# Kernel tuning notes

Measured on AMD Instinct MI355X. Metric: run time of the kernel, lower is better.

Reference implementation:

```python
import jax, jax.numpy as jnp
import numpy as np
from jax import lax

SCALE = 4          # pansharpening ratio (init arg)
K = 31             # kornia BoxBlur((31,31))
PAD = K // 2
EPS = 1e-10
R_EXP = 4          # r in the paper
A_W = 1.0          # a weight on loss_a


def box_blur(x):
    # x: [B,1,H,W]; normalized 31x31 box filter with reflect padding
    # (kornia BoxBlur default border_type='reflect'), done separably.
    xp = jnp.pad(x, ((0, 0), (0, 0), (PAD, PAD), (PAD, PAD)), mode='reflect')
    kv = jnp.ones((1, 1, K, 1), x.dtype) / K
    kh = jnp.ones((1, 1, 1, K), x.dtype) / K
    dn = ('NCHW', 'OIHW', 'NCHW')
    y = lax.conv_general_dilated(xp, kv, (1, 1), 'VALID', dimension_numbers=dn)
    return lax.conv_general_dilated(y, kh, (1, 1), 'VALID', dimension_numbers=dn)


def setup_inputs() -> dict:
    key = jax.random.key(0)
    k1, k2, k3, k4 = jax.random.split(key, 4)
    B, C, H, W = 4, 8, 1024, 1024
    h, w = H // SCALE, W // SCALE
    return {
        'lr_ms':   jax.random.uniform(k1, (B, C, h, w), jnp.float32),
        'hr_pan':  jax.random.uniform(k2, (B, 1, H, W), jnp.float32),
        'hr_ms':   jax.random.uniform(k3, (B, C, H, W), jnp.float32),
        'fuse_ms': jax.random.uniform(k4, (B, C, H, W), jnp.float32),
    }


def reference(lr_ms, hr_pan, hr_ms, fuse_ms):
    B, C, h, w = lr_ms.shape
    H, W = hr_pan.shape[2], hr_pan.shape[3]

    # F.upsample(mode='area', scale_factor=1/SCALE) == SCALE x SCALE average pool
    dp = hr_pan.reshape(B, 1, H // SCALE, SCALE, W // SCALE, SCALE).mean(axis=(3, 5))
    b = dp.reshape(B, -1)                                   # [B, N]

    # Batched lstsq: A = [1, lr_ms bands]^T per sample, solve via normal eqs
    ones = jnp.ones((B, 1, h * w), lr_ms.dtype)
    A = jnp.concatenate([ones, lr_ms.reshape(B, C, -1)], axis=1)   # [B, C+1, N]
    AtA = jnp.einsum('bcn,bdn->bcd', A, A)                  # [B, C+1, C+1]
    Atb = jnp.einsum('bcn,bn->bc', A, b)                    # [B, C+1]
    sol = jnp.linalg.solve(AtA, Atb[..., None])[..., 0]     # [B, C+1]

    # Synthetic intensity images M_ (from GT hr_ms) and G_ (from fused output)
    bias = sol[:, 0][:, None, None]
    M_ = (bias + jnp.einsum('bc,bchw->bhw', sol[:, 1:], hr_ms))[:, None]    # [B,1,H,W]
    G_ = (bias + jnp.einsum('bc,bchw->bhw', sol[:, 1:], fuse_ms))[:, None]  # [B,1,H,W]

    mean_M = box_blur(M_)
    mean_P = box_blur(hr_pan)
    cov_MP = box_blur(M_ * hr_pan) - mean_M * mean_P
    std_M = jnp.sqrt(jnp.abs(box_blur(M_ * M_) - mean_M * mean_M) + EPS)
    std_P = jnp.sqrt(jnp.abs(box_blur(hr_pan * hr_pan) - mean_P * mean_P) + EPS)
    S = (cov_MP / (std_M * std_P)) ** R_EXP                 # [B,1,H,W], broadcasts over C

    loss_c = jnp.mean(jnp.abs(fuse_ms * S - hr_ms * S))

    grad_P = (hr_pan - mean_P) / std_P
    mean_G = box_blur(G_)
    std_G = jnp.sqrt(jnp.abs(box_blur(G_ * G_) - mean_G * mean_G) + EPS)
    grad_G = (G_ - mean_G) / std_G
    loss_a = jnp.mean(jnp.abs(grad_G * (2 - S) - grad_P * (2 - S)))

    return loss_c + A_W * loss_a
```

## Files before the change

### kernel.cpp

```cpp
#include <hip/hip_runtime.h>
#include <math.h>

#define HW_IMG (1u<<20)
#define W_ 1024
#define H_ 1024
#define B_ 4
#define C_ 8
#define N_LR 65536

__device__ __forceinline__ int refl1024(int i){
  if(i<0) i=-i;
  if(i>1023) i=2046-i;
  return i;
}

__global__ __launch_bounds__(256) void k_fit(const float* __restrict__ lr_ms,
                                             const float* __restrict__ hr_pan,
                                             double* __restrict__ atab){
  int b = blockIdx.y;
  int tid = blockIdx.x*256 + threadIdx.x;
  float acc[54];
  #pragma unroll
  for(int i=0;i<54;i++) acc[i]=0.f;
  const float* pan = hr_pan + (size_t)b*HW_IMG;
  const float* lr  = lr_ms + (size_t)b*C_*N_LR;
  for(int k=0;k<4;k++){
    int n = tid*4+k;
    int i = n>>8, j = n&255;
    float s=0.f;
    #pragma unroll
    for(int dy=0;dy<4;dy++){
      const float* pr = pan + (size_t)(i*4+dy)*W_ + j*4;
      s += pr[0]+pr[1]+pr[2]+pr[3];
    }
    float bv = s*(1.f/16.f);
    float a[9];
    a[0]=1.f;
    #pragma unroll
    for(int c=0;c<C_;c++) a[c+1]=lr[(size_t)c*N_LR + n];
    int idx=0;
    #pragma unroll
    for(int p=0;p<9;p++){
      #pragma unroll
      for(int q=p;q<9;q++){ acc[idx] = fmaf(a[p],a[q],acc[idx]); idx++; }
    }
    #pragma unroll
    for(int p=0;p<9;p++) acc[45+p] = fmaf(a[p],bv,acc[45+p]);
  }
  #pragma unroll
  for(int v=0;v<54;v++){
    float x = acc[v];
    for(int off=32;off>0;off>>=1) x += __shfl_down(x, off, 64);
    if((threadIdx.x & 63)==0) atomicAdd(&atab[b*54+v], (double)x);
  }
}

__global__ void k_solve(const double* __restrict__ atab, double* __restrict__ sol){
  int b = threadIdx.x;
  if(b>=B_) return;
  double A[9][10];
  const double* src = atab + b*54;
  int idx=0;
  for(int p=0;p<9;p++)
    for(int q=p;q<9;q++){ A[p][q]=src[idx]; A[q][p]=src[idx]; idx++; }
  for(int p=0;p<9;p++) A[p][9]=src[45+p];
  for(int col=0; col<9; col++){
    int piv=col; double mx=fabs(A[col][col]);
    for(int r=col+1;r<9;r++){ double v=fabs(A[r][col]); if(v>mx){mx=v;piv=r;} }
    if(piv!=col){
      for(int c2=col;c2<10;c2++){ double t=A[col][c2]; A[col][c2]=A[piv][c2]; A[piv][c2]=t; }
    }
    double inv = 1.0/A[col][col];
    for(int r=col+1;r<9;r++){
      double f = A[r][col]*inv;
      for(int c2=col;c2<10;c2++) A[r][c2] -= f*A[col][c2];
    }
  }
  double x[9];
  for(int r=8;r>=0;r--){
    double s=A[r][9];
    for(int c2=r+1;c2<9;c2++) s -= A[r][c2]*x[c2];
    x[r]=s/A[r][r];
  }
  for(int i=0;i<9;i++) sol[b*9+i]=x[i];
}

__global__ __launch_bounds__(256) void k_synth(const float* __restrict__ hr_ms,
                                               const float* __restrict__ fuse_ms,
                                               const double* __restrict__ sol,
                                               float* __restrict__ M,
                                               float* __restrict__ G,
                                               float* __restrict__ D){
  size_t t = (size_t)blockIdx.x*256 + threadIdx.x;
  int b = (int)(t >> 18);
  size_t pix = (t & (size_t)((1<<18)-1))*4;
  const double* s = sol + b*9;
  float bias = (float)s[0];
  float4 m = {bias,bias,bias,bias};
  float4 g = m;
  float4 d = {0.f,0.f,0.f,0.f};
  #pragma unroll
  for(int c=0;c<C_;c++){
    float w = (float)s[c+1];
    size_t off = (((size_t)b*C_ + c)<<20) + pix;
    float4 hv = *(const float4*)(hr_ms+off);
    float4 fv = *(const float4*)(fuse_ms+off);
    m.x=fmaf(w,hv.x,m.x); m.y=fmaf(w,hv.y,m.y); m.z=fmaf(w,hv.z,m.z); m.w=fmaf(w,hv.w,m.w);
    g.x=fmaf(w,fv.x,g.x); g.y=fmaf(w,fv.y,g.y); g.z=fmaf(w,fv.z,g.z); g.w=fmaf(w,fv.w,g.w);
    d.x+=fabsf(fv.x-hv.x); d.y+=fabsf(fv.y-hv.y); d.z+=fabsf(fv.z-hv.z); d.w+=fabsf(fv.w-hv.w);
  }
  size_t p = ((size_t)b<<20) + pix;
  *(float4*)(M+p)=m; *(float4*)(G+p)=g; *(float4*)(D+p)=d;
}

__global__ __launch_bounds__(256) void k_vblur(const float* __restrict__ M,
                                               const float* __restrict__ P,
                                               const float* __restrict__ G,
                                               float* __restrict__ VB){
  int x  = blockIdx.x*256 + threadIdx.x;
  int b  = blockIdx.y;
  int y0 = blockIdx.z * 16;
  const float* Mp = M + (size_t)b*HW_IMG;
  const float* Pp = P + (size_t)b*HW_IMG;
  const float* Gp = G + (size_t)b*HW_IMG;
  float S0=0,S1=0,S2=0,S3=0,S4=0,S5=0,S6=0;
  #define TAPV(yy, op) { int r = refl1024(yy); size_t off=(size_t)r*W_+x; \
    float mv=Mp[off], pv=Pp[off], gv=Gp[off]; \
    S0 op mv; S1 op pv; S2 op mv*pv; S3 op mv*mv; S4 op pv*pv; S5 op gv; S6 op gv*gv; }
  for(int k=y0-15;k<=y0+15;k++) TAPV(k, +=);
  const float inv = 1.f/31.f;
  size_t base = (size_t)b*HW_IMG + (size_t)y0*W_ + x;
  const size_t CH = (size_t)B_*HW_IMG;
  for(int i=0;i<16;i++){
    size_t o = base + (size_t)i*W_;
    VB[o]      = S0*inv; VB[CH+o]   = S1*inv; VB[2*CH+o] = S2*inv;
    VB[3*CH+o] = S3*inv; VB[4*CH+o] = S4*inv; VB[5*CH+o] = S5*inv;
    VB[6*CH+o] = S6*inv;
    if(i<15){
      int y = y0+i;
      TAPV(y+16, +=);
      TAPV(y-15, -=);
    }
  }
  #undef TAPV
}

#define LIDX(i) ((i)+((i)>>5))
__global__ __launch_bounds__(128) void k_hfinal(const float* __restrict__ VB,
                                                const float* __restrict__ P,
                                                const float* __restrict__ G,
                                                const float* __restrict__ D,
                                                double* __restrict__ partial){
  __shared__ float lds[7*1056];
  __shared__ float red[4];
  int row = blockIdx.x;
  int b = row>>10, y = row&1023;
  int t = threadIdx.x;
  size_t rowoff = (size_t)b*HW_IMG + (size_t)y*W_;
  const size_t CH = (size_t)B_*HW_IMG;
  for(int ch=0; ch<7; ch++){
    const float* src = VB + (size_t)ch*CH + rowoff;
    float* dst = lds + ch*1056;
    for(int i=t*4; i<1024; i+=512){
      float4 v = *(const float4*)(src+i);
      dst[LIDX(i)]   = v.x;
      dst[LIDX(i+1)] = v.y;
      dst[LIDX(i+2)] = v.z;
      dst[LIDX(i+3)] = v.w;
    }
  }
  int x0 = t*8;
  float pv[8], gv[8], dv[8];
  {
    const float* Pr = P + rowoff + x0;
    const float* Gr = G + rowoff + x0;
    const float* Dr = D + rowoff + x0;
    #pragma unroll
    for(int i=0;i<2;i++){
      float4 a = *(const float4*)(Pr + i*4);
      pv[i*4]=a.x; pv[i*4+1]=a.y; pv[i*4+2]=a.z; pv[i*4+3]=a.w;
      float4 c = *(const float4*)(Gr + i*4);
      gv[i*4]=c.x; gv[i*4+1]=c.y; gv[i*4+2]=c.z; gv[i*4+3]=c.w;
      float4 e = *(const float4*)(Dr + i*4);
      dv[i*4]=e.x; dv[i*4+1]=e.y; dv[i*4+2]=e.z; dv[i*4+3]=e.w;
    }
  }
  __syncthreads();
  float S[7];
  #pragma unroll
  for(int ch=0;ch<7;ch++) S[ch]=0.f;
  #define TAPH(xx, op) { int r=refl1024(xx); int li=LIDX(r); \
    S[0] op lds[li];        S[1] op lds[1056+li];   S[2] op lds[2*1056+li]; \
    S[3] op lds[3*1056+li]; S[4] op lds[4*1056+li]; S[5] op lds[5*1056+li]; \
    S[6] op lds[6*1056+li]; }
  for(int k=x0-15;k<=x0+15;k++) TAPH(k, +=);
  const float inv = 1.f/31.f;
  float lc=0.f, la=0.f;
  #pragma unroll
  for(int i=0;i<8;i++){
    float mM=S[0]*inv, mP=S[1]*inv, mMP=S[2]*inv, mMM=S[3]*inv,
          mPP=S[4]*inv, mG=S[5]*inv, mGG=S[6]*inv;
    float cov  = mMP - mM*mP;
    float stdM = sqrtf(fabsf(mMM - mM*mM)+1e-10f);
    float stdP = sqrtf(fabsf(mPP - mP*mP)+1e-10f);
    float stdG = sqrtf(fabsf(mGG - mG*mG)+1e-10f);
    float corr = cov/(stdM*stdP);
    float c2 = corr*corr;
    float S4v = c2*c2;
    float gradP = (pv[i]-mP)/stdP;
    float gradG = (gv[i]-mG)/stdG;
    lc += dv[i]*S4v;
    la += fabsf((gradG-gradP)*(2.f-S4v));
    if(i<7){
      int x = x0+i;
      TAPH(x+16, +=);
      TAPH(x-15, -=);
    }
  }
  #undef TAPH
  for(int off=32;off>0;off>>=1){
    lc += __shfl_down(lc, off, 64);
    la += __shfl_down(la, off, 64);
  }
  int wid = t>>6;
  if((t&63)==0){ red[wid*2]=lc; red[wid*2+1]=la; }
  __syncthreads();
  if(t==0){
    partial[(size_t)row*2]   = (double)red[0]+(double)red[2];
    partial[(size_t)row*2+1] = (double)red[1]+(double)red[3];
  }
}

__global__ __launch_bounds__(256) void k_out(const double* __restrict__ partial,
                                             float* __restrict__ out){
  int t = threadIdx.x;
  double lc=0.0, la=0.0;
  for(int i=t;i<4096;i+=256){ lc+=partial[2*i]; la+=partial[2*i+1]; }
  for(int off=32;off>0;off>>=1){
    lc += __shfl_down(lc, off, 64);
    la += __shfl_down(la, off, 64);
  }
  __shared__ double red[8];
  int wid = t>>6;
  if((t&63)==0){ red[wid*2]=lc; red[wid*2+1]=la; }
  __syncthreads();
  if(t==0){
    double c = red[0]+red[2]+red[4]+red[6];
    double a = red[1]+red[3]+red[5]+red[7];
    out[0] = (float)(c*(1.0/33554432.0) + a*(1.0/4194304.0));
  }
}

extern "C" void kernel_launch(void* const* d_in, const int* in_sizes, int n_in,
                              void* d_out, int out_size, void* d_ws, size_t ws_size,
                              hipStream_t stream){
  const float* lr_ms   = (const float*)d_in[0];
  const float* hr_pan  = (const float*)d_in[1];
  const float* hr_ms   = (const float*)d_in[2];
  const float* fuse_ms = (const float*)d_in[3];
  float* out = (float*)d_out;

  char* ws = (char*)d_ws;
  double* atab    = (double*)ws;
  double* sol     = (double*)(ws + 4096);
  double* partial = (double*)(ws + 8192);
  float* M  = (float*)(ws + 131072);
  float* G  = M + (size_t)B_*HW_IMG;
  float* Dd = G + (size_t)B_*HW_IMG;
  float* VB = Dd + (size_t)B_*HW_IMG;

  hipMemsetAsync(d_ws, 0, 4096, stream);
  k_fit  <<<dim3(64,4),   256, 0, stream>>>(lr_ms, hr_pan, atab);
  k_solve<<<1,            64,  0, stream>>>(atab, sol);
  k_synth<<<4096,         256, 0, stream>>>(hr_ms, fuse_ms, sol, M, G, Dd);
  k_vblur<<<dim3(4,4,64), 256, 0, stream>>>(M, hr_pan, G, VB);
  k_hfinal<<<4096,        128, 0, stream>>>(VB, hr_pan, G, Dd, partial);
  k_out  <<<1, 256, 0, stream>>>(partial, out);
}
```

Baseline: 460.3 us.

## Fuse vertical and horizontal box blur into one kernel via LDS row staging

Merges the vertical-blur kernel and the horizontal-blur/loss kernel into a single kernel. Each block runs a sliding vertical window over 8 rows with float4 loads, stages two rows of seven blurred channels in shared memory, then applies the horizontal blur and loss reduction directly. This removes the 7-channel intermediate VB buffer written to and read back from global memory. The synth kernel is also restructured so each thread loops over all batches. The fused grid has only 512 blocks, so there is less parallelism, and each vertical sweep repeats a 30-row warm-up per 8 output rows.

```diff
diff --git a/kernel.cpp b/kernel.cpp
--- a/kernel.cpp
+++ b/kernel.cpp
@@ -91,133 +91,130 @@
                                                float* __restrict__ M,
                                                float* __restrict__ G,
                                                float* __restrict__ D){
-  size_t t = (size_t)blockIdx.x*256 + threadIdx.x;
-  int b = (int)(t >> 18);
-  size_t pix = (t & (size_t)((1<<18)-1))*4;
-  const double* s = sol + b*9;
-  float bias = (float)s[0];
-  float4 m = {bias,bias,bias,bias};
-  float4 g = m;
-  float4 d = {0.f,0.f,0.f,0.f};
+  size_t pix = ((size_t)blockIdx.x*256 + threadIdx.x)*4;
   #pragma unroll
-  for(int c=0;c<C_;c++){
-    float w = (float)s[c+1];
-    size_t off = (((size_t)b*C_ + c)<<20) + pix;
-    float4 hv = *(const float4*)(hr_ms+off);
-    float4 fv = *(const float4*)(fuse_ms+off);
-    m.x=fmaf(w,hv.x,m.x); m.y=fmaf(w,hv.y,m.y); m.z=fmaf(w,hv.z,m.z); m.w=fmaf(w,hv.w,m.w);
-    g.x=fmaf(w,fv.x,g.x); g.y=fmaf(w,fv.y,g.y); g.z=fmaf(w,fv.z,g.z); g.w=fmaf(w,fv.w,g.w);
-    d.x+=fabsf(fv.x-hv.x); d.y+=fabsf(fv.y-hv.y); d.z+=fabsf(fv.z-hv.z); d.w+=fabsf(fv.w-hv.w);
-  }
-  size_t p = ((size_t)b<<20) + pix;
-  *(float4*)(M+p)=m; *(float4*)(G+p)=g; *(float4*)(D+p)=d;
-}
-
-__global__ __launch_bounds__(256) void k_vblur(const float* __restrict__ M,
-                                               const float* __restrict__ P,
-                                               const float* __restrict__ G,
-                                               float* __restrict__ VB){
-  int x  = blockIdx.x*256 + threadIdx.x;
+  for(int b=0;b<B_;b++){
+    const double* s = sol + b*9;
+    float bias = (float)s[0];
+    float4 m = {bias,bias,bias,bias};
+    float4 g = m;
+    float4 d = {0.f,0.f,0.f,0.f};
+    #pragma unroll
+    for(int c=0;c<C_;c++){
+      float w = (float)s[c+1];
+      size_t off = (((size_t)(b*C_+c))<<20) + pix;
+      float4 hv = *(const float4*)(hr_ms+off);
+      float4 fv = *(const float4*)(fuse_ms+off);
+      m.x=fmaf(w,hv.x,m.x); m.y=fmaf(w,hv.y,m.y); m.z=fmaf(w,hv.z,m.z); m.w=fmaf(w,hv.w,m.w);
+      g.x=fmaf(w,fv.x,g.x); g.y=fmaf(w,fv.y,g.y); g.z=fmaf(w,fv.z,g.z); g.w=fmaf(w,fv.w,g.w);
+      d.x+=fabsf(fv.x-hv.x); d.y+=fabsf(fv.y-hv.y);
+      d.z+=fabsf(fv.z-hv.z); d.w+=fabsf(fv.w-hv.w);
+    }
+    size_t p = ((size_t)b<<20) + pix;
+    *(float4*)(M+p)=m; *(float4*)(G+p)=g; *(float4*)(D+p)=d;
+  }
+}
+
+#define LIDX(i) ((i)+((i)>>5))
+#define ACC4(S, V, op) { S.x op V.x; S.y op V.y; S.z op V.z; S.w op V.w; }
+__global__ __launch_bounds__(256) void k_vh(const float* __restrict__ M,
+                                            const float* __restrict__ P,
+                                            const float* __restrict__ G,
+                                            const float* __restrict__ D,
+                                            double* __restrict__ partial){
+  __shared__ float vs[2][7][1056];
+  __shared__ float red[8];
+  int t  = threadIdx.x;
+  int y0 = blockIdx.x*8;
   int b  = blockIdx.y;
-  int y0 = blockIdx.z * 16;
   const float* Mp = M + (size_t)b*HW_IMG;
   const float* Pp = P + (size_t)b*HW_IMG;
   const float* Gp = G + (size_t)b*HW_IMG;
-  float S0=0,S1=0,S2=0,S3=0,S4=0,S5=0,S6=0;
-  #define TAPV(yy, op) { int r = refl1024(yy); size_t off=(size_t)r*W_+x; \
-    float mv=Mp[off], pv=Pp[off], gv=Gp[off]; \
-    S0 op mv; S1 op pv; S2 op mv*pv; S3 op mv*mv; S4 op pv*pv; S5 op gv; S6 op gv*gv; }
-  for(int k=y0-15;k<=y0+15;k++) TAPV(k, +=);
+  int x4 = t*4;
   const float inv = 1.f/31.f;
-  size_t base = (size_t)b*HW_IMG + (size_t)y0*W_ + x;
-  const size_t CH = (size_t)B_*HW_IMG;
-  for(int i=0;i<16;i++){
-    size_t o = base + (size_t)i*W_;
-    VB[o]      = S0*inv; VB[CH+o]   = S1*inv; VB[2*CH+o] = S2*inv;
-    VB[3*CH+o] = S3*inv; VB[4*CH+o] = S4*inv; VB[5*CH+o] = S5*inv;
-    VB[6*CH+o] = S6*inv;
-    if(i<15){
-      int y = y0+i;
-      TAPV(y+16, +=);
-      TAPV(y-15, -=);
-    }
+
+  float4 S0={0,0,0,0},S1=S0,S2=S0,S3=S0,S4=S0,S5=S0,S6=S0;
+  #define TAPV(yy, op) { int r_ = refl1024(yy); size_t off=(size_t)r_*W_+x4; \
+    float4 mv=*(const float4*)(Mp+off); \
+    float4 pv_=*(const float4*)(Pp+off); \
+    float4 gv_=*(const float4*)(Gp+off); \
+    ACC4(S0,mv,op) ACC4(S1,pv_,op) \
+    { float4 tq={mv.x*pv_.x,mv.y*pv_.y,mv.z*pv_.z,mv.w*pv_.w}; ACC4(S2,tq,op) } \
+    { float4 tq={mv.x*mv.x,mv.y*mv.y,mv.z*mv.z,mv.w*mv.w}; ACC4(S3,tq,op) } \
+    { float4 tq={pv_.x*pv_.x,pv_.y*pv_.y,pv_.z*pv_.z,pv_.w*pv_.w}; ACC4(S4,tq,op) } \
+    ACC4(S5,gv_,op) \
+    { float4 tq={gv_.x*gv_.x,gv_.y*gv_.y,gv_.z*gv_.z,gv_.w*gv_.w}; ACC4(S6,tq,op) } }
+
+  for(int k=y0-15;k<y0+15;k++) TAPV(k, +=);
+
+  float lc=0.f, la=0.f;
+  int xh = (t&127)*8;
+  int rsel = t>>7;
+
+  for(int stage=0; stage<4; stage++){
+    #pragma unroll
+    for(int rr=0; rr<2; rr++){
+      int r = y0 + stage*2 + rr;
+      TAPV(r+15, +=);
+      #define STV(ch, S) { float* dst = &vs[rr][ch][0]; \
+        dst[LIDX(x4)]  =S.x*inv; dst[LIDX(x4+1)]=S.y*inv; \
+        dst[LIDX(x4+2)]=S.z*inv; dst[LIDX(x4+3)]=S.w*inv; }
+      STV(0,S0) STV(1,S1) STV(2,S2) STV(3,S3) STV(4,S4) STV(5,S5) STV(6,S6)
+      #undef STV
+      TAPV(r-15, -=);
+    }
+    __syncthreads();
+    int rh = y0 + stage*2 + rsel;
+    size_t rowoff = (size_t)b*HW_IMG + (size_t)rh*W_;
+    float pv[8], gv[8], dv[8];
+    {
+      const float* Pr = Pp + (size_t)rh*W_ + xh;
+      const float* Gr = Gp + (size_t)rh*W_ + xh;
+      const float* Dr = D + rowoff + xh;
+      #pragma unroll
+      for(int i=0;i<2;i++){
+        float4 a = *(const float4*)(Pr + i*4);
+        pv[i*4]=a.x; pv[i*4+1]=a.y; pv[i*4+2]=a.z; pv[i*4+3]=a.w;
+        float4 c = *(const float4*)(Gr + i*4);
+        gv[i*4]=c.x; gv[i*4+1]=c.y; gv[i*4+2]=c.z; gv[i*4+3]=c.w;
+        float4 e = *(const float4*)(Dr + i*4);
+        dv[i*4]=e.x; dv[i*4+1]=e.y; dv[i*4+2]=e.z; dv[i*4+3]=e.w;
+      }
+    }
+    float Wc[7];
+    #pragma unroll
+    for(int ch=0;ch<7;ch++) Wc[ch]=0.f;
+    #define TAPH(xx, op) { int r_=refl1024(xx); int li=LIDX(r_); \
+      Wc[0] op vs[rsel][0][li]; Wc[1] op vs[rsel][1][li]; Wc[2] op vs[rsel][2][li]; \
+      Wc[3] op vs[rsel][3][li]; Wc[4] op vs[rsel][4][li]; Wc[5] op vs[rsel][5][li]; \
+      Wc[6] op vs[rsel][6][li]; }
+    for(int k=xh-15;k<=xh+15;k++) TAPH(k, +=);
+    #pragma unroll
+    for(int i=0;i<8;i++){
+      float mM=Wc[0]*inv, mP=Wc[1]*inv, mMP=Wc[2]*inv, mMM=Wc[3]*inv,
+            mPP=Wc[4]*inv, mG=Wc[5]*inv, mGG=Wc[6]*inv;
+      float cov  = mMP - mM*mP;
+      float stdM = sqrtf(fabsf(mMM - mM*mM)+1e-10f);
+      float stdP = sqrtf(fabsf(mPP - mP*mP)+1e-10f);
+      float stdG = sqrtf(fabsf(mGG - mG*mG)+1e-10f);
+      float corr = cov/(stdM*stdP);
+      float c2 = corr*corr;
+      float S4v = c2*c2;
+      float gradP = (pv[i]-mP)/stdP;
+      float gradG = (gv[i]-mG)/stdG;
+      lc += dv[i]*S4v;
+      la += fabsf((gradG-gradP)*(2.f-S4v));
+      if(i<7){
+        int x = xh+i;
+        TAPH(x+16, +=);
+        TAPH(x-15, -=);
+      }
+    }
+    #undef TAPH
+    __syncthreads();
   }
   #undef TAPV
-}
-
-#define LIDX(i) ((i)+((i)>>5))
-__global__ __launch_bounds__(128) void k_hfinal(const float* __restrict__ VB,
-                                                const float* __restrict__ P,
-                                                const float* __restrict__ G,
-                                                const float* __restrict__ D,
-                                                double* __restrict__ partial){
-  __shared__ float lds[7*1056];
-  __shared__ float red[4];
-  int row = blockIdx.x;
-  int b = row>>10, y = row&1023;
-  int t = threadIdx.x;
-  size_t rowoff = (size_t)b*HW_IMG + (size_t)y*W_;
-  const size_t CH = (size_t)B_*HW_IMG;
-  for(int ch=0; ch<7; ch++){
-    const float* src = VB + (size_t)ch*CH + rowoff;
-    float* dst = lds + ch*1056;
-    for(int i=t*4; i<1024; i+=512){
-      float4 v = *(const float4*)(src+i);
-      dst[LIDX(i)]   = v.x;
-      dst[LIDX(i+1)] = v.y;
-      dst[LIDX(i+2)] = v.z;
-      dst[LIDX(i+3)] = v.w;
-    }
-  }
-  int x0 = t*8;
-  float pv[8], gv[8], dv[8];
-  {
-    const float* Pr = P + rowoff + x0;
-    const float* Gr = G + rowoff + x0;
-    const float* Dr = D + rowoff + x0;
-    #pragma unroll
-    for(int i=0;i<2;i++){
-      float4 a = *(const float4*)(Pr + i*4);
-      pv[i*4]=a.x; pv[i*4+1]=a.y; pv[i*4+2]=a.z; pv[i*4+3]=a.w;
-      float4 c = *(const float4*)(Gr + i*4);
-      gv[i*4]=c.x; gv[i*4+1]=c.y; gv[i*4+2]=c.z; gv[i*4+3]=c.w;
-      float4 e = *(const float4*)(Dr + i*4);
-      dv[i*4]=e.x; dv[i*4+1]=e.y; dv[i*4+2]=e.z; dv[i*4+3]=e.w;
-    }
-  }
-  __syncthreads();
-  float S[7];
-  #pragma unroll
-  for(int ch=0;ch<7;ch++) S[ch]=0.f;
-  #define TAPH(xx, op) { int r=refl1024(xx); int li=LIDX(r); \
-    S[0] op lds[li];        S[1] op lds[1056+li];   S[2] op lds[2*1056+li]; \
-    S[3] op lds[3*1056+li]; S[4] op lds[4*1056+li]; S[5] op lds[5*1056+li]; \
-    S[6] op lds[6*1056+li]; }
-  for(int k=x0-15;k<=x0+15;k++) TAPH(k, +=);
-  const float inv = 1.f/31.f;
-  float lc=0.f, la=0.f;
-  #pragma unroll
-  for(int i=0;i<8;i++){
-    float mM=S[0]*inv, mP=S[1]*inv, mMP=S[2]*inv, mMM=S[3]*inv,
-          mPP=S[4]*inv, mG=S[5]*inv, mGG=S[6]*inv;
-    float cov  = mMP - mM*mP;
-    float stdM = sqrtf(fabsf(mMM - mM*mM)+1e-10f);
-    float stdP = sqrtf(fabsf(mPP - mP*mP)+1e-10f);
-    float stdG = sqrtf(fabsf(mGG - mG*mG)+1e-10f);
-    float corr = cov/(stdM*stdP);
-    float c2 = corr*corr;
-    float S4v = c2*c2;
-    float gradP = (pv[i]-mP)/stdP;
-    float gradG = (gv[i]-mG)/stdG;
-    lc += dv[i]*S4v;
-    la += fabsf((gradG-gradP)*(2.f-S4v));
-    if(i<7){
-      int x = x0+i;
-      TAPH(x+16, +=);
-      TAPH(x-15, -=);
-    }
-  }
-  #undef TAPH
+
   for(int off=32;off>0;off>>=1){
     lc += __shfl_down(lc, off, 64);
     la += __shfl_down(la, off, 64);
@@ -226,8 +223,9 @@
   if((t&63)==0){ red[wid*2]=lc; red[wid*2+1]=la; }
   __syncthreads();
   if(t==0){
-    partial[(size_t)row*2]   = (double)red[0]+(double)red[2];
-    partial[(size_t)row*2+1] = (double)red[1]+(double)red[3];
+    int blk = blockIdx.y*gridDim.x + blockIdx.x;
+    partial[(size_t)blk*2]   = (double)red[0]+(double)red[2]+(double)red[4]+(double)red[6];
+    partial[(size_t)blk*2+1] = (double)red[1]+(double)red[3]+(double)red[5]+(double)red[7];
   }
 }
 
@@ -235,7 +233,7 @@
                                              float* __restrict__ out){
   int t = threadIdx.x;
   double lc=0.0, la=0.0;
-  for(int i=t;i<4096;i+=256){ lc+=partial[2*i]; la+=partial[2*i+1]; }
+  for(int i=t;i<512;i+=256){ lc+=partial[2*i]; la+=partial[2*i+1]; }
   for(int off=32;off>0;off>>=1){
     lc += __shfl_down(lc, off, 64);
     la += __shfl_down(la, off, 64);
@@ -267,13 +265,11 @@
   float* M  = (float*)(ws + 131072);
   float* G  = M + (size_t)B_*HW_IMG;
   float* Dd = G + (size_t)B_*HW_IMG;
-  float* VB = Dd + (size_t)B_*HW_IMG;
 
   hipMemsetAsync(d_ws, 0, 4096, stream);
   k_fit  <<<dim3(64,4),   256, 0, stream>>>(lr_ms, hr_pan, atab);
   k_solve<<<1,            64,  0, stream>>>(atab, sol);
-  k_synth<<<4096,         256, 0, stream>>>(hr_ms, fuse_ms, sol, M, G, Dd);
-  k_vblur<<<dim3(4,4,64), 256, 0, stream>>>(M, hr_pan, G, VB);
-  k_hfinal<<<4096,        128, 0, stream>>>(VB, hr_pan, G, Dd, partial);
+  k_synth<<<1024,         256, 0, stream>>>(hr_ms, fuse_ms, sol, M, G, Dd);
+  k_vh   <<<dim3(128,4),  256, 0, stream>>>(M, hr_pan, G, Dd, partial);
   k_out  <<<1, 256, 0, stream>>>(partial, out);
 }
```

New measurement: 432.7 us. 6.0% less time.
